# Kernel tuning notes

Hardware: AMD Instinct MI355X
Metric: run time of the kernel (lower is better)

## Reference

```python
import jax, jax.numpy as jnp
import numpy as np

KH, KW = 3, 3  # spatial kernel from kernel_size=(1,3,3,C)


def _extract_patches_valid(x, kh, kw):
    # TF extract_image_patches ordering: depth = (row, col, channel) flattened.
    B, H, W, C = x.shape
    Ho, Wo = H - kh + 1, W - kw + 1
    # stack kh*kw shifted views -> [B, Ho, Wo, kh*kw, C]
    views = [x[:, i:i + Ho, j:j + Wo, :] for i in range(kh) for j in range(kw)]
    patches = jnp.stack(views, axis=3)
    return patches.reshape(B, Ho, Wo, kh * kw * C)


def setup_inputs() -> dict:
    key = jax.random.key(0)
    k1, k2, k3 = jax.random.split(key, 3)
    B, H, W, C = 32, 112, 112, 32
    filters = 128
    patch_dim = KH * KW * C  # 288
    x = jax.random.normal(k1, (B, H, W, C), dtype=jnp.float32)
    ccs = jax.random.uniform(k2, (patch_dim, filters), dtype=jnp.float32)  # RandomUniform(0,1)
    beta = jax.random.uniform(k3, (filters,), dtype=jnp.float32)
    return {"x": x, "ccs": ccs, "beta": beta}


def reference(x, ccs, beta):
    B = x.shape[0]
    patch_dim, filters = ccs.shape
    patches = _extract_patches_valid(x, KH, KW)  # [B, Ho, Wo, patch_dim]
    Ho, Wo = patches.shape[1], patches.shape[2]
    p = patches.reshape(B, Ho * Wo, patch_dim)  # [B, P, D]
    # squared distance: ||p||^2 - 2 p.ccs + ||ccs||^2  -> [B, P, filters]
    p_sq = jnp.sum(p * p, axis=2, keepdims=True)
    c_sq = jnp.sum(ccs * ccs, axis=0, keepdims=True)
    scores = p_sq - 2.0 * jnp.einsum('bpd,df->bpf', p, ccs) + c_sq
    out = jnp.exp(-beta * scores)  # RBF activation, beta broadcast over filters
    return out.reshape(B, Ho, Wo, filters)
```

## Files before the change

kernel.cpp:

```cpp
#include <hip/hip_runtime.h>


typedef __attribute__((ext_vector_type(8))) short bf16x8;
typedef __attribute__((ext_vector_type(4))) float f32x4;

#define HH 112
#define WW 112
#define CC 32
#define HO 110
#define WO 110
#define NF 128
#define KD 288
#define RPX 114
#define XP 40

__device__ __forceinline__ unsigned short f32_to_bf16(float f) {
    unsigned u = __float_as_uint(f);
    unsigned r = u + 0x7FFFu + ((u >> 16) & 1u);
    return (unsigned short)(r >> 16);
}

__global__ __launch_bounds__(256) void rbf_prologue(const float* __restrict__ ccs,
                                                    unsigned short* __restrict__ ccs_t,
                                                    float* __restrict__ c_sq) {
    int idx = blockIdx.x * 256 + threadIdx.x;
    int d = idx >> 7;
    int f = idx & 127;
    float v = ccs[idx];
    ccs_t[f * KD + d] = f32_to_bf16(v);
    atomicAdd(&c_sq[f], v * v);
}

__global__ __launch_bounds__(256) void rbf_main(const float* __restrict__ x,
                                                const unsigned short* __restrict__ ccs_t,
                                                const float* __restrict__ c_sq,
                                                const float* __restrict__ beta,
                                                float* __restrict__ out) {
    __shared__ unsigned short xs[4 * RPX * XP];
    __shared__ float colsum[456];
    __shared__ float p_sq[2 * 112];

    const int t = threadIdx.x;
    const int y0 = blockIdx.x * 2;
    const int b = blockIdx.y;

    const float* xbase = x + (size_t)((b * HH + y0) * WW) * CC;

    #pragma unroll
    for (int p = 0; p < 14; ++p) {
        int idx = t + p * 256;
        int q = idx & 7;
        int ic = idx >> 3;
        int col = ic % 112;
        int i = ic / 112;
        const float4 v = *(const float4*)(xbase + (i * WW + col) * CC + q * 4);
        unsigned short h0 = f32_to_bf16(v.x), h1 = f32_to_bf16(v.y);
        unsigned short h2 = f32_to_bf16(v.z), h3 = f32_to_bf16(v.w);
        uint2 pk;
        pk.x = (unsigned)h0 | ((unsigned)h1 << 16);
        pk.y = (unsigned)h2 | ((unsigned)h3 << 16);
        *(uint2*)(&xs[(i * RPX + col) * XP + q * 4]) = pk;
        float part = v.x * v.x + v.y * v.y + v.z * v.z + v.w * v.w;
        part += __shfl_xor(part, 1);
        part += __shfl_xor(part, 2);
        part += __shfl_xor(part, 4);
        if (q == 0) colsum[ic] = part;
    }
    __syncthreads();

    if (t < 224) {
        int r = (t >= 112) ? 1 : 0;
        int c = t - r * 112;
        float s = 0.f;
        #pragma unroll
        for (int i = 0; i < 3; ++i)
            #pragma unroll
            for (int j = 0; j < 3; ++j)
                s += colsum[(r + i) * 112 + c + j];
        p_sq[t] = s;
    }
    __syncthreads();

    const int lane  = t & 63;
    const int wave  = t >> 6;
    const int laneM = lane & 15;
    const int quad  = lane >> 4;

    const unsigned short* ap0 = ccs_t + (size_t)(wave * 32 + laneM) * KD + quad * 8;
    const unsigned short* ap1 = ap0 + 16 * KD;

    const int fb = wave * 32 + quad * 4;
    const float4 cs0 = *(const float4*)(c_sq + fb);
    const float4 cs1 = *(const float4*)(c_sq + fb + 16);
    const float4 bt0 = *(const float4*)(beta + fb);
    const float4 bt1 = *(const float4*)(beta + fb + 16);

    #pragma unroll
    for (int r = 0; r < 2; ++r) {
        f32x4 acc[7][2];
        #pragma unroll
        for (int mi = 0; mi < 7; ++mi) {
            acc[mi][0] = (f32x4){0.f, 0.f, 0.f, 0.f};
            acc[mi][1] = (f32x4){0.f, 0.f, 0.f, 0.f};
        }

        #pragma unroll
        for (int kb = 0; kb < 9; ++kb) {
            const int ki = kb / 3, kj = kb % 3;
            bf16x8 a0 = *(const bf16x8*)(ap0 + kb * 32);
            bf16x8 a1 = *(const bf16x8*)(ap1 + kb * 32);
            #pragma unroll
            for (int mi = 0; mi < 7; ++mi) {
                const bf16x8 bf = *(const bf16x8*)(&xs[((r + ki) * RPX + mi * 16 + laneM + kj) * XP + quad * 8]);
                acc[mi][0] = __builtin_amdgcn_mfma_f32_16x16x32_bf16(a0, bf, acc[mi][0], 0, 0, 0);
                acc[mi][1] = __builtin_amdgcn_mfma_f32_16x16x32_bf16(a1, bf, acc[mi][1], 0, 0, 0);
            }
        }

        float* orow = out + (size_t)((b * HO + y0 + r) * WO) * NF;
        #pragma unroll
        for (int mi = 0; mi < 7; ++mi) {
            const int px = mi * 16 + laneM;
            const float ps = p_sq[r * 112 + px];
            float* op = orow + (size_t)px * NF + fb;
            #pragma unroll
            for (int ft = 0; ft < 2; ++ft) {
                const float4 cs = ft ? cs1 : cs0;
                const float4 bt = ft ? bt1 : bt0;
                float4 o;
                o.x = __expf(-bt.x * (ps - 2.f * acc[mi][ft][0] + cs.x));
                o.y = __expf(-bt.y * (ps - 2.f * acc[mi][ft][1] + cs.y));
                o.z = __expf(-bt.z * (ps - 2.f * acc[mi][ft][2] + cs.z));
                o.w = __expf(-bt.w * (ps - 2.f * acc[mi][ft][3] + cs.w));
                if (px < WO)
                    *(float4*)(op + ft * 16) = o;
            }
        }
    }
}

extern "C" void kernel_launch(void* const* d_in, const int* in_sizes, int n_in,
                              void* d_out, int out_size, void* d_ws, size_t ws_size,
                              hipStream_t stream) {
    const float* x    = (const float*)d_in[0];
    const float* ccs  = (const float*)d_in[1];
    const float* beta = (const float*)d_in[2];
    float* out = (float*)d_out;

    unsigned short* ccs_t = (unsigned short*)d_ws;
    float* c_sq = (float*)((char*)d_ws + 128 * KD * sizeof(unsigned short));

    hipMemsetAsync(c_sq, 0, NF * sizeof(float), stream);
    rbf_prologue<<<144, 256, 0, stream>>>(ccs, ccs_t, c_sq);
    rbf_main<<<dim3(55, 32), 256, 0, stream>>>(x, ccs_t, c_sq, beta, out);
}
```

Baseline: 287.4 us.

## Process four output rows per block and compute c_sq without atomics

Each block now loads six input rows and produces four output rows instead of two, which cuts the redundant halo loads and bf16 conversion of overlapping rows. The last block handles a partial tile by clamping rows. The LDS row pitch shrinks from 40 to 32 halfwords, which may cause bank conflicts on the MFMA B-fragment reads. The prologue replaces the memset plus atomicAdd with a serial per-filter sum in block 0, which lengthens the prologue's critical path. The grid halves to 28x32 blocks, leaving fewer blocks than before to spread across the CUs.

Result: faster. 269.4 us (-6.2%).

```diff
diff --git a/kernel.cpp b/kernel.cpp
--- a/kernel.cpp
+++ b/kernel.cpp
@@ -12,7 +12,7 @@
 #define NF 128
 #define KD 288
 #define RPX 114
-#define XP 40
+#define XP 32
 
 __device__ __forceinline__ unsigned short f32_to_bf16(float f) {
     unsigned u = __float_as_uint(f);
@@ -26,9 +26,17 @@
     int idx = blockIdx.x * 256 + threadIdx.x;
     int d = idx >> 7;
     int f = idx & 127;
-    float v = ccs[idx];
-    ccs_t[f * KD + d] = f32_to_bf16(v);
-    atomicAdd(&c_sq[f], v * v);
+    ccs_t[f * KD + d] = f32_to_bf16(ccs[idx]);
+    if (blockIdx.x == 0 && threadIdx.x < 128) {
+        const int fc = threadIdx.x;
+        float s = 0.f;
+        #pragma unroll 8
+        for (int dd = 0; dd < KD; ++dd) {
+            float v = ccs[dd * NF + fc];
+            s += v * v;
+        }
+        c_sq[fc] = s;
+    }
 }
 
 __global__ __launch_bounds__(256) void rbf_main(const float* __restrict__ x,
@@ -36,24 +44,24 @@
                                                 const float* __restrict__ c_sq,
                                                 const float* __restrict__ beta,
                                                 float* __restrict__ out) {
-    __shared__ unsigned short xs[4 * RPX * XP];
-    __shared__ float colsum[456];
-    __shared__ float p_sq[2 * 112];
+    __shared__ unsigned short xs[6 * RPX * XP];
+    __shared__ float colsum[676];
+    __shared__ float p_sq[4 * 112];
 
     const int t = threadIdx.x;
-    const int y0 = blockIdx.x * 2;
+    const int y0 = blockIdx.x * 4;
     const int b = blockIdx.y;
-
-    const float* xbase = x + (size_t)((b * HH + y0) * WW) * CC;
+    const int rows = (HO - y0 < 4) ? (HO - y0) : 4;
 
     #pragma unroll
-    for (int p = 0; p < 14; ++p) {
+    for (int p = 0; p < 21; ++p) {
         int idx = t + p * 256;
         int q = idx & 7;
         int ic = idx >> 3;
         int col = ic % 112;
         int i = ic / 112;
-        const float4 v = *(const float4*)(xbase + (i * WW + col) * CC + q * 4);
+        int yg = y0 + i; if (yg > HH - 1) yg = HH - 1;
+        const float4 v = *(const float4*)(x + ((size_t)(b * HH + yg) * WW + col) * CC + q * 4);
         unsigned short h0 = f32_to_bf16(v.x), h1 = f32_to_bf16(v.y);
         unsigned short h2 = f32_to_bf16(v.z), h3 = f32_to_bf16(v.w);
         uint2 pk;
@@ -68,16 +76,20 @@
     }
     __syncthreads();
 
-    if (t < 224) {
-        int r = (t >= 112) ? 1 : 0;
-        int c = t - r * 112;
-        float s = 0.f;
-        #pragma unroll
-        for (int i = 0; i < 3; ++i)
+    #pragma unroll
+    for (int pp = 0; pp < 2; ++pp) {
+        int idx = t + pp * 256;
+        if (idx < 448) {
+            int r = idx / 112;
+            int c = idx - r * 112;
+            float s = 0.f;
             #pragma unroll
-            for (int j = 0; j < 3; ++j)
-                s += colsum[(r + i) * 112 + c + j];
-        p_sq[t] = s;
+            for (int i = 0; i < 3; ++i)
+                #pragma unroll
+                for (int j = 0; j < 3; ++j)
+                    s += colsum[(r + i) * 112 + c + j];
+            p_sq[idx] = s;
+        }
     }
     __syncthreads();
 
@@ -95,8 +107,7 @@
     const float4 bt0 = *(const float4*)(beta + fb);
     const float4 bt1 = *(const float4*)(beta + fb + 16);
 
-    #pragma unroll
-    for (int r = 0; r < 2; ++r) {
+    for (int r = 0; r < rows; ++r) {
         f32x4 acc[7][2];
         #pragma unroll
         for (int mi = 0; mi < 7; ++mi) {
@@ -150,7 +161,6 @@
     unsigned short* ccs_t = (unsigned short*)d_ws;
     float* c_sq = (float*)((char*)d_ws + 128 * KD * sizeof(unsigned short));
 
-    hipMemsetAsync(c_sq, 0, NF * sizeof(float), stream);
     rbf_prologue<<<144, 256, 0, stream>>>(ccs, ccs_t, c_sq);
-    rbf_main<<<dim3(55, 32), 256, 0, stream>>>(x, ccs_t, c_sq, beta, out);
+    rbf_main<<<dim3(28, 32), 256, 0, stream>>>(x, ccs_t, c_sq, beta, out);
 }
```
